# Kernel optimization log

Measured on AMD Instinct MI355X. Metric: run time of the kernel, lower is better.

## Reference

```python
import jax, jax.numpy as jnp
import numpy as np
from functools import partial

N_NODES = 10000
E_EDGES = 160000
SEQ = 32
IN_CH = 128
HID = 64
HEADS = 8
GRU_H = 256
NEG_SLOPE = 0.2


def setup_inputs() -> dict:
    key = jax.random.key(0)
    ks = jax.random.split(key, 24)
    x = jax.random.normal(ks[0], (SEQ, N_NODES, IN_CH), dtype=jnp.float32)
    edge_attr = jax.random.normal(ks[1], (E_EDGES, 3), dtype=jnp.float32)
    edge_src = jax.random.randint(ks[2], (E_EDGES,), 0, N_NODES, dtype=jnp.int32)
    # guarantee no self loops (PyG removes then re-adds them; we add them in reference)
    off = jax.random.randint(ks[3], (E_EDGES,), 1, N_NODES, dtype=jnp.int32)
    edge_dst = (edge_src + off) % N_NODES
    s = 0.05
    p = {}
    # gat1: in -> heads*hid
    p['gat1_wl'] = jax.random.normal(ks[4], (IN_CH, HEADS * HID)) * s
    p['gat1_wr'] = jax.random.normal(ks[5], (IN_CH, HEADS * HID)) * s
    p['gat1_we'] = jax.random.normal(ks[6], (3, HEADS * HID)) * s
    p['gat1_att'] = jax.random.normal(ks[7], (HEADS, HID)) * s
    p['gat1_b'] = jnp.zeros((HEADS * HID,), jnp.float32)
    # gat2: heads*hid -> 1*hid
    p['gat2_wl'] = jax.random.normal(ks[8], (HEADS * HID, HID)) * s
    p['gat2_wr'] = jax.random.normal(ks[9], (HEADS * HID, HID)) * s
    p['gat2_we'] = jax.random.normal(ks[10], (3, HID)) * s
    p['gat2_att'] = jax.random.normal(ks[11], (1, HID)) * s
    p['gat2_b'] = jnp.zeros((HID,), jnp.float32)
    # GRU layer 0, forward and backward directions (only layer 0 affects the output)
    p['gru_wih_f'] = jax.random.normal(ks[12], (3 * GRU_H, HID)) * s
    p['gru_whh_f'] = jax.random.normal(ks[13], (3 * GRU_H, GRU_H)) * s
    p['gru_bih_f'] = jnp.zeros((3 * GRU_H,), jnp.float32)
    p['gru_bhh_f'] = jnp.zeros((3 * GRU_H,), jnp.float32)
    p['gru_wih_b'] = jax.random.normal(ks[14], (3 * GRU_H, HID)) * s
    p['gru_whh_b'] = jax.random.normal(ks[15], (3 * GRU_H, GRU_H)) * s
    p['gru_bih_b'] = jnp.zeros((3 * GRU_H,), jnp.float32)
    p['gru_bhh_b'] = jnp.zeros((3 * GRU_H,), jnp.float32)
    p['fc_w'] = jax.random.normal(ks[16], (33, 2 * GRU_H)) * s
    p['fc_b'] = jnp.zeros((33,), jnp.float32)
    return dict(x=x, edge_attr=edge_attr, edge_src=edge_src, edge_dst=edge_dst, **p)


def _gatv2(x, src, dst, e_emb, wl, wr, att, b, n_nodes):
    # x: [N, F_in]; e_emb: [E_full, H, C]; att: [H, C]
    H, C = att.shape
    xl = (x @ wl).reshape(n_nodes, H, C)
    xr = (x @ wr).reshape(n_nodes, H, C)
    m = jax.nn.leaky_relu(xl[src] + xr[dst] + e_emb, NEG_SLOPE)  # [E, H, C]
    logits = jnp.einsum('ehc,hc->eh', m, att)                    # [E, H]
    mx = jax.ops.segment_max(logits, dst, num_segments=n_nodes)
    ex = jnp.exp(logits - mx[dst])
    den = jax.ops.segment_sum(ex, dst, num_segments=n_nodes)
    alpha = ex / den[dst]
    out = jax.ops.segment_sum(alpha[:, :, None] * xl[src], dst, num_segments=n_nodes)
    return out.reshape(n_nodes, H * C) + b


def _gru_scan(seq, wih, whh, bih, bhh):
    # seq: [T, N, F]; returns final hidden [N, GRU_H]
    Hh = whh.shape[1]
    def cell(h, x_t):
        gi = x_t @ wih.T + bih
        gh = h @ whh.T + bhh
        ir, iz, inn = jnp.split(gi, 3, axis=-1)
        hr, hz, hn = jnp.split(gh, 3, axis=-1)
        r = jax.nn.sigmoid(ir + hr)
        z = jax.nn.sigmoid(iz + hz)
        n = jnp.tanh(inn + r * hn)
        h = (1.0 - z) * n + z * h
        return h, None
    h0 = jnp.zeros((seq.shape[1], Hh), seq.dtype)
    hT, _ = jax.lax.scan(cell, h0, seq)
    return hT


def reference(x, edge_attr, edge_src, edge_dst,
              gat1_wl, gat1_wr, gat1_we, gat1_att, gat1_b,
              gat2_wl, gat2_wr, gat2_we, gat2_att, gat2_b,
              gru_wih_f, gru_whh_f, gru_bih_f, gru_bhh_f,
              gru_wih_b, gru_whh_b, gru_bih_b, gru_bhh_b,
              fc_w, fc_b):
    T, N, _ = x.shape
    E = edge_src.shape[0]
    loop = jnp.arange(N, dtype=edge_src.dtype)
    src = jnp.concatenate([edge_src, loop])
    dst = jnp.concatenate([edge_dst, loop])
    # self-loop edge attr = mean of incoming edge attrs (PyG fill_value='mean')
    deg = jax.ops.segment_sum(jnp.ones((E,), x.dtype), edge_dst, num_segments=N)
    loop_attr = jax.ops.segment_sum(edge_attr, edge_dst, num_segments=N) / jnp.maximum(deg, 1.0)[:, None]
    ea = jnp.concatenate([edge_attr, loop_attr], axis=0)  # [E+N, 3]
    e1 = (ea @ gat1_we).reshape(-1, HEADS, HID)
    e2 = (ea @ gat2_we).reshape(-1, 1, HID)

    @jax.checkpoint
    def step(carry, x_t):
        h1 = jax.nn.elu(_gatv2(x_t, src, dst, e1, gat1_wl, gat1_wr, gat1_att, gat1_b, N))
        h2 = jax.nn.elu(_gatv2(h1, src, dst, e2, gat2_wl, gat2_wr, gat2_att, gat2_b, N))
        return carry, h2

    _, emb = jax.lax.scan(step, 0, x)  # [T, N, HID]

    # torch code uses h_n[0] (layer-0 fwd final) and h_n[1] (layer-0 bwd final);
    # deeper GRU layers do not influence the output.
    hf = _gru_scan(emb, gru_wih_f, gru_whh_f, gru_bih_f, gru_bhh_f)
    hb = _gru_scan(emb[::-1], gru_wih_b, gru_whh_b, gru_bih_b, gru_bhh_b)
    comb = jnp.concatenate([hf, hb], axis=1)           # [N, 512]
    g = jnp.mean(comb, axis=0, keepdims=True)          # [1, 512]
    return g @ fc_w.T + fc_b                           # [1, 33]
```

## Files before the change

kernel.cpp:

```cpp
#include <hip/hip_runtime.h>

#define T_SEQ   32
#define N_NODES 10000
#define E_EDGES 160000
#define EF      (E_EDGES + N_NODES)
#define IN_CH   128
#define HID     64
#define HEADS   8
#define HC      512
#define GRU_H   256
#define G3      768

typedef __attribute__((ext_vector_type(8))) short short8;
typedef __attribute__((ext_vector_type(4))) float f32x4;
typedef unsigned short ushort_t;

__device__ __forceinline__ float wave_reduce_sum(float v){
#pragma unroll
  for (int off = 32; off; off >>= 1) v += __shfl_xor(v, off, 64);
  return v;
}

__device__ __forceinline__ ushort_t f2bf(float v){
  unsigned u = __float_as_uint(v);
  unsigned r = u + 0x7FFFu + ((u >> 16) & 1u);
  return (ushort_t)(r >> 16);
}
__device__ __forceinline__ float bf2f(ushort_t b){
  return __uint_as_float(((unsigned)b) << 16);
}

__device__ __forceinline__ void async_cp16(const void* g, void* l){
  __builtin_amdgcn_global_load_lds((const __attribute__((address_space(1))) void*)g,
                                   (__attribute__((address_space(3))) void*)l, 16, 0, 0);
}


__global__ __launch_bounds__(256)
void deg_loop_kernel(const int* __restrict__ edst, const float* __restrict__ eattr,
                     int* __restrict__ deg, float* __restrict__ lsum){
  int e = blockIdx.x * 256 + threadIdx.x;
  if (e < E_EDGES){
    int d = edst[e];
    atomicAdd(&deg[d], 1);
    atomicAdd(&lsum[d*3+0], eattr[e*3+0]);
    atomicAdd(&lsum[d*3+1], eattr[e*3+1]);
    atomicAdd(&lsum[d*3+2], eattr[e*3+2]);
  }
}

__global__ __launch_bounds__(256)
void loop_div_kernel(const int* __restrict__ deg, const float* __restrict__ lsum,
                     float* __restrict__ lattr){
  int n = blockIdx.x * 256 + threadIdx.x;
  if (n < N_NODES){
    float d = fmaxf((float)deg[n], 1.0f);
    lattr[n*3+0] = lsum[n*3+0] / d;
    lattr[n*3+1] = lsum[n*3+1] / d;
    lattr[n*3+2] = lsum[n*3+2] / d;
  }
}

__global__ __launch_bounds__(256)
void scan_rowptr_kernel(const int* __restrict__ deg, int* __restrict__ row_ptr){
  __shared__ int sums[256];
  __shared__ int base[256];
  int tid = threadIdx.x;
  const int CH = 40;
  int start = tid * CH;
  int s = 0;
  for (int k = 0; k < CH; k++){
    int n = start + k;
    if (n < N_NODES) s += deg[n];
  }
  sums[tid] = s;
  __syncthreads();
  if (tid == 0){
    int acc = 0;
    for (int i = 0; i < 256; i++){ base[i] = acc; acc += sums[i]; }
  }
  __syncthreads();
  int acc = base[tid];
  for (int k = 0; k < CH; k++){
    int n = start + k;
    if (n < N_NODES){ row_ptr[n] = acc; acc += deg[n]; }
    else if (n == N_NODES){ row_ptr[n] = acc; }
  }
}

__global__ __launch_bounds__(256)
void csr_fill_kernel(const int* __restrict__ edst, const int* __restrict__ row_ptr,
                     int* __restrict__ cursor, int* __restrict__ col){
  int e = blockIdx.x * 256 + threadIdx.x;
  if (e < E_EDGES){
    int d = edst[e];
    int pos = row_ptr[d] + atomicAdd(&cursor[d], 1);
    col[pos] = e;
  }
}

__global__ __launch_bounds__(256)
void build_emeta(const float* __restrict__ eattr, const float* __restrict__ lattr,
                 const int* __restrict__ esrc, float4* __restrict__ emeta){
  int e = blockIdx.x * 256 + threadIdx.x;
  if (e < E_EDGES){
    emeta[e] = make_float4(eattr[e*3], eattr[e*3+1], eattr[e*3+2], __int_as_float(esrc[e]));
  } else if (e < EF){
    int n = e - E_EDGES;
    emeta[e] = make_float4(lattr[n*3], lattr[n*3+1], lattr[n*3+2], __int_as_float(n));
  }
}


__global__ __launch_bounds__(256)
void split_arr4(const float4* __restrict__ src, ushort4* __restrict__ hi,
                ushort4* __restrict__ lo, long n4){
  long idx = (long)blockIdx.x * 256 + threadIdx.x;
  if (idx < n4){
    float4 v = src[idx];
    float vv[4] = {v.x, v.y, v.z, v.w};
    ushort4 h, l;
    ushort_t* hp = (ushort_t*)&h; ushort_t* lp = (ushort_t*)&l;
#pragma unroll
    for (int i = 0; i < 4; i++){
      ushort_t hh = f2bf(vv[i]);
      hp[i] = hh; lp[i] = f2bf(vv[i] - bf2f(hh));
    }
    hi[idx] = h; lo[idx] = l;
  }
}

__global__ __launch_bounds__(256)
void split_w_gat1(const float* __restrict__ wl, const float* __restrict__ wr,
                  ushort_t* __restrict__ hi, ushort_t* __restrict__ lo){
  int idx = blockIdx.x * 256 + threadIdx.x;
  if (idx >= 1024 * 128) return;
  int n = idx >> 7, k = idx & 127;
  float v = (n < 512) ? wl[k * 512 + n] : wr[k * 512 + (n - 512)];
  ushort_t h = f2bf(v);
  hi[idx] = h; lo[idx] = f2bf(v - bf2f(h));
}

__global__ __launch_bounds__(256)
void split_w_gat2(const float* __restrict__ wl, const float* __restrict__ wr,
                  ushort_t* __restrict__ hi, ushort_t* __restrict__ lo){
  int idx = blockIdx.x * 256 + threadIdx.x;
  if (idx >= 128 * 512) return;
  int n = idx >> 9, k = idx & 511;
  float v = (n < 64) ? wl[k * 64 + n] : wr[k * 64 + (n - 64)];
  ushort_t h = f2bf(v);
  hi[idx] = h; lo[idx] = f2bf(v - bf2f(h));
}

__global__ __launch_bounds__(256)
void pack_w_gru(const float* __restrict__ wih, const float* __restrict__ whh,
                ushort_t* __restrict__ hi, ushort_t* __restrict__ lo){
  int idx = blockIdx.x * 256 + threadIdx.x;
  if (idx >= 4 * 10 * 192 * 32) return;
  int kk = idx & 31;
  int r  = (idx >> 5) % 192;
  int kc = (idx >> 5) / 192 % 10;
  int jt = idx / (32 * 192 * 10);
  int g = r >> 6, jj = r & 63;
  int wrow = g * 256 + jt * 64 + jj;
  int k = kc * 32 + kk;
  float v = (k < 64) ? wih[wrow * 64 + k] : whh[wrow * 256 + (k - 64)];
  ushort_t h = f2bf(v);
  hi[idx] = h; lo[idx] = f2bf(v - bf2f(h));
}


__global__ __launch_bounds__(256)
void gemm_nolds(const ushort_t* __restrict__ Ah, const ushort_t* __restrict__ Al,
                const ushort_t* __restrict__ Bh, const ushort_t* __restrict__ Bl,
                float* __restrict__ C, int M, int K, int N){
  int tid = threadIdx.x;
  int w = tid >> 6, lane = tid & 63;
  int m16 = lane & 15, quad = lane >> 4;
  int n0 = (blockIdx.y * 4 + w) * 64;
  if (n0 >= N) return;
  int m0 = blockIdx.x * 32;

  f32x4 acc[2][4];
#pragma unroll
  for (int i = 0; i < 2; i++)
#pragma unroll
    for (int j = 0; j < 4; j++) acc[i][j] = (f32x4){0,0,0,0};

  int ar0 = m0 + m16;      if (ar0 >= M) ar0 = M - 1;
  int ar1 = m0 + 16 + m16; if (ar1 >= M) ar1 = M - 1;
  const ushort_t* Ah0 = Ah + (size_t)ar0 * K + quad * 8;
  const ushort_t* Al0 = Al + (size_t)ar0 * K + quad * 8;
  const ushort_t* Ah1 = Ah + (size_t)ar1 * K + quad * 8;
  const ushort_t* Al1 = Al + (size_t)ar1 * K + quad * 8;

  for (int k0 = 0; k0 < K; k0 += 32){
    short8 a_h[2], a_l[2];
    a_h[0] = *(const short8*)(Ah0 + k0); a_l[0] = *(const short8*)(Al0 + k0);
    a_h[1] = *(const short8*)(Ah1 + k0); a_l[1] = *(const short8*)(Al1 + k0);
#pragma unroll
    for (int nt = 0; nt < 4; nt++){
      size_t boff = (size_t)(n0 + nt * 16 + m16) * K + k0 + quad * 8;
      short8 b_h = *(const short8*)(Bh + boff);
      short8 b_l = *(const short8*)(Bl + boff);
#pragma unroll
      for (int mt = 0; mt < 2; mt++){
        acc[mt][nt] = __builtin_amdgcn_mfma_f32_16x16x32_bf16(a_h[mt], b_h, acc[mt][nt],0,0,0);
        acc[mt][nt] = __builtin_amdgcn_mfma_f32_16x16x32_bf16(a_h[mt], b_l, acc[mt][nt],0,0,0);
        acc[mt][nt] = __builtin_amdgcn_mfma_f32_16x16x32_bf16(a_l[mt], b_h, acc[mt][nt],0,0,0);
      }
    }
  }
#pragma unroll
  for (int mt = 0; mt < 2; mt++){
    int row = m0 + mt * 16 + quad * 4;
#pragma unroll
    for (int nt = 0; nt < 4; nt++){
      int cc = n0 + nt * 16 + m16;
#pragma unroll
      for (int r4 = 0; r4 < 4; r4++){
        if (row + r4 < M) C[(size_t)(row + r4) * N + cc] = acc[mt][nt][r4];
      }
    }
  }
}

__global__ __launch_bounds__(256)
void gemm1_swz(const ushort_t* __restrict__ Ah, const ushort_t* __restrict__ Al,
               const ushort_t* __restrict__ Bh, const ushort_t* __restrict__ Bl,
               float* __restrict__ C){
  const int M = N_NODES, K = IN_CH, N = 1024;
  int bid = blockIdx.x;
  int xcd = bid & 7, lk = bid >> 3;
  int wsw = (xcd < 4 ? xcd * 157 : 628 + (xcd - 4) * 156) + lk;
  int mb = wsw >> 2, nbq = wsw & 3;

  int tid = threadIdx.x;
  int w = tid >> 6, lane = tid & 63;
  int m16 = lane & 15, quad = lane >> 4;
  int n0 = (nbq * 4 + w) * 64;
  int m0 = mb * 32;

  f32x4 acc[2][4];
#pragma unroll
  for (int i = 0; i < 2; i++)
#pragma unroll
    for (int j = 0; j < 4; j++) acc[i][j] = (f32x4){0,0,0,0};

  int ar0 = m0 + m16;      if (ar0 >= M) ar0 = M - 1;
  int ar1 = m0 + 16 + m16; if (ar1 >= M) ar1 = M - 1;
  const ushort_t* Ah0 = Ah + (size_t)ar0 * K + quad * 8;
  const ushort_t* Al0 = Al + (size_t)ar0 * K + quad * 8;
  const ushort_t* Ah1 = Ah + (size_t)ar1 * K + quad * 8;
  const ushort_t* Al1 = Al + (size_t)ar1 * K + quad * 8;

  for (int k0 = 0; k0 < K; k0 += 32){
    short8 a_h[2], a_l[2];
    a_h[0] = *(const short8*)(Ah0 + k0); a_l[0] = *(const short8*)(Al0 + k0);
    a_h[1] = *(const short8*)(Ah1 + k0); a_l[1] = *(const short8*)(Al1 + k0);
#pragma unroll
    for (int nt = 0; nt < 4; nt++){
      size_t boff = (size_t)(n0 + nt * 16 + m16) * K + k0 + quad * 8;
      short8 b_h = *(const short8*)(Bh + boff);
      short8 b_l = *(const short8*)(Bl + boff);
#pragma unroll
      for (int mt = 0; mt < 2; mt++){
        acc[mt][nt] = __builtin_amdgcn_mfma_f32_16x16x32_bf16(a_h[mt], b_h, acc[mt][nt],0,0,0);
        acc[mt][nt] = __builtin_amdgcn_mfma_f32_16x16x32_bf16(a_h[mt], b_l, acc[mt][nt],0,0,0);
        acc[mt][nt] = __builtin_amdgcn_mfma_f32_16x16x32_bf16(a_l[mt], b_h, acc[mt][nt],0,0,0);
      }
    }
  }
#pragma unroll
  for (int mt = 0; mt < 2; mt++){
    int row = m0 + mt * 16 + quad * 4;
#pragma unroll
    for (int nt = 0; nt < 4; nt++){
      int cc = n0 + nt * 16 + m16;
#pragma unroll
      for (int r4 = 0; r4 < 4; r4++){
        if (row + r4 < M) C[(size_t)(row + r4) * N + cc] = acc[mt][nt][r4];
      }
    }
  }
}


struct GruArgs {
  const ushort_t *EtH[2], *EtL[2];
  const ushort_t *WpH[2], *WpL[2];
  const float    *BIH[2], *BHH[2];
  const ushort_t *HinH[2],*HinL[2];
  ushort_t *HoutH[2], *HoutL[2];
  int first;
};

#define GRU_STAGE(BB, AH, AL, ASTRIDE, ACOL, KC)                               \
  {                                                                            \
    _Pragma("unroll")                                                          \
    for (int pass = 0; pass < 2; pass++){                                      \
      int ch = pass * 256 + tid;             \
      int lch = ch ^ ((ch >> 3) & 7);              \
      int row = lch >> 2, c = (lch & 3) * 8;                                   \
      int anode = m0 + row; if (anode >= N_NODES) anode = N_NODES - 1;         \
      async_cp16(AH + (size_t)anode * ASTRIDE + (ACOL) + c, &Ah_s[BB][ch * 8]);\
      async_cp16(AL + (size_t)anode * ASTRIDE + (ACOL) + c, &Al_s[BB][ch * 8]);\
    }                                                                          \
    const ushort_t* bh = WpH + ((size_t)jt * 10 + (KC)) * 6144;                \
    const ushort_t* bl = WpL + ((size_t)jt * 10 + (KC)) * 6144;                \
    _Pragma("unroll")                                                          \
    for (int pass = 0; pass < 3; pass++){                                      \
      int ch = pass * 256 + tid;             \
      int lch = ch ^ ((ch >> 3) & 7);                                          \
      async_cp16(bh + lch * 8, &Bh_s[BB][ch * 8]);                             \
      async_cp16(bl + lch * 8, &Bl_s[BB][ch * 8]);                             \
    }                                                                          \
  }

#define GRU_COMPUTE(BB, NTGT)                                                  \
  {                                                                            \
    short8 a_h[4], a_l[4];                                                     \
    _Pragma("unroll")                                                          \
    for (int mt = 0; mt < 4; mt++){                                            \
      int r = wm * 64 + mt * 16 + m16;                                         \
      int so = ((r * 4 + quad) ^ ((r >> 1) & 7)) * 8;                          \
      a_h[mt] = *(const short8*)&Ah_s[BB][so];                                 \
      a_l[mt] = *(const short8*)&Al_s[BB][so];                                 \
    }                                                                          \
    _Pragma("unroll")                                                          \
    for (int g = 0; g < 3; g++){                                               \
      int tgt = (g < 2) ? g : (NTGT);                                          \
      _Pragma("unroll")                                                        \
      for (int nt = 0; nt < 2; nt++){                                          \
        int r = g * 64 + wn * 32 + nt * 16 + m16;                              \
        int so = ((r * 4 + quad) ^ ((r >> 1) & 7)) * 8;                        \
        short8 b_h = *(const short8*)&Bh_s[BB][so];                            \
        short8 b_l = *(const short8*)&Bl_s[BB][so];                            \
        _Pragma("unroll")                                                      \
        for (int mt = 0; mt < 4; mt++){                                        \
          acc[tgt][mt][nt] = __builtin_amdgcn_mfma_f32_16x16x32_bf16(a_h[mt], b_h, acc[tgt][mt][nt],0,0,0); \
          acc[tgt][mt][nt] = __builtin_amdgcn_mfma_f32_16x16x32_bf16(a_h[mt], b_l, acc[tgt][mt][nt],0,0,0); \
          acc[tgt][mt][nt] = __builtin_amdgcn_mfma_f32_16x16x32_bf16(a_l[mt], b_h, acc[tgt][mt][nt],0,0,0); \
        }                                                                      \
      }                                                                        \
    }                                                                          \
  }

__global__ __launch_bounds__(256, 2)
void gru_step(GruArgs ga){
  int bid = blockIdx.x;
  int wsw = (bid & 7) * 79 + (bid >> 3);
  int m0 = (wsw >> 3) * 128;
  int sub = wsw & 7;
  int jt = sub >> 1;
  int dir = sub & 1;

  const ushort_t* EtH  = ga.EtH[dir];  const ushort_t* EtL  = ga.EtL[dir];
  const ushort_t* WpH  = ga.WpH[dir];  const ushort_t* WpL  = ga.WpL[dir];
  const float*    BIH  = ga.BIH[dir];  const float*    BHH  = ga.BHH[dir];
  const ushort_t* HinH = ga.HinH[dir]; const ushort_t* HinL = ga.HinL[dir];
  ushort_t* HoutH = ga.HoutH[dir];     ushort_t* HoutL = ga.HoutL[dir];

  __shared__ __align__(16) short Ah_s[2][128 * 32];
  __shared__ __align__(16) short Al_s[2][128 * 32];
  __shared__ __align__(16) short Bh_s[2][192 * 32];
  __shared__ __align__(16) short Bl_s[2][192 * 32];

  int tid = threadIdx.x;
  int w = tid >> 6, lane = tid & 63;
  int wm = w >> 1, wn = w & 1;
  int m16 = lane & 15, quad = lane >> 4;
  int j0 = jt * 64;

  f32x4 acc[4][4][2];
#pragma unroll
  for (int g = 0; g < 4; g++)
#pragma unroll
    for (int i = 0; i < 4; i++)
#pragma unroll
      for (int j = 0; j < 2; j++) acc[g][i][j] = (f32x4){0,0,0,0};

  GRU_STAGE(0, EtH, EtL, 64, 0, 0)
  __syncthreads();
  GRU_STAGE(1, EtH, EtL, 64, 32, 1)
  GRU_COMPUTE(0, 2)
  __syncthreads();
  if (!ga.first){
    GRU_STAGE(0, HinH, HinL, 256, 0, 2)
    GRU_COMPUTE(1, 2)
    __syncthreads();
    for (int kc = 2; kc < 9; kc++){
      GRU_STAGE((kc + 1) & 1, HinH, HinL, 256, (kc - 1) * 32, kc + 1)
      GRU_COMPUTE(kc & 1, 3)
      __syncthreads();
    }
    GRU_COMPUTE(1, 3)
  } else {
    GRU_COMPUTE(1, 2)
  }

#pragma unroll
  for (int mt = 0; mt < 4; mt++){
    int row = m0 + wm * 64 + mt * 16 + quad * 4;
#pragma unroll
    for (int nt = 0; nt < 2; nt++){
      int j = j0 + wn * 32 + nt * 16 + m16;
      float br  = BIH[j] + BHH[j];
      float bz  = BIH[GRU_H + j] + BHH[GRU_H + j];
      float bni = BIH[2*GRU_H + j];
      float bnh = BHH[2*GRU_H + j];
#pragma unroll
      for (int r4 = 0; r4 < 4; r4++){
        int node = row + r4;
        if (node < N_NODES){
          float rr = 1.f / (1.f + __expf(-(acc[0][mt][nt][r4] + br)));
          float zz = 1.f / (1.f + __expf(-(acc[1][mt][nt][r4] + bz)));
          float nn = tanhf(acc[2][mt][nt][r4] + bni + rr * (acc[3][mt][nt][r4] + bnh));
          size_t hidx = (size_t)node * GRU_H + j;
          float hold = ga.first ? 0.f : (bf2f(HinH[hidx]) + bf2f(HinL[hidx]));
          float hv = (1.f - zz) * nn + zz * hold;
          ushort_t hh = f2bf(hv);
          HoutH[hidx] = hh;
          HoutL[hidx] = f2bf(hv - bf2f(hh));
        }
      }
    }
  }
}


__device__ __forceinline__ void gat1_half(float4 xl, float4 xr,
                                          float a0, float a1, float a2,
                                          float4 we0, float4 we1, float4 we2,
                                          float4 at, bool valid,
                                          float& den, float4& acc){
  float vx = xl.x + xr.x + a0*we0.x + a1*we1.x + a2*we2.x;
  float vy = xl.y + xr.y + a0*we0.y + a1*we1.y + a2*we2.y;
  float vz = xl.z + xr.z + a0*we0.z + a1*we1.z + a2*we2.z;
  float vw = xl.w + xr.w + a0*we0.w + a1*we1.w + a2*we2.w;
  vx = fmaxf(vx, 0.2f*vx); vy = fmaxf(vy, 0.2f*vy);
  vz = fmaxf(vz, 0.2f*vz); vw = fmaxf(vw, 0.2f*vw);
  float pm = vx*at.x + vy*at.y + vz*at.z + vw*at.w;
  pm += __shfl_xor(pm, 1, 64); pm += __shfl_xor(pm, 2, 64);
  pm += __shfl_xor(pm, 4, 64); pm += __shfl_xor(pm, 8, 64);
  float wgt = valid ? __expf(pm) : 0.f;
  den += wgt;
  acc.x += wgt * xl.x; acc.y += wgt * xl.y;
  acc.z += wgt * xl.z; acc.w += wgt * xl.w;
}

__global__ __launch_bounds__(256)
void gat1_fused(const float* __restrict__ xlr, const float4* __restrict__ emeta,
                const int* __restrict__ row_ptr, const int* __restrict__ col,
                const float* __restrict__ we, const float* __restrict__ att,
                const float* __restrict__ bias,
                ushort_t* __restrict__ outh, ushort_t* __restrict__ outl){
  int n = (blockIdx.x * 256 + threadIdx.x) >> 6;
  int lane = threadIdx.x & 63;
  if (n >= N_NODES) return;
  int ch0 = lane * 4;
  int ch1 = 256 + lane * 4;

  float4 att0 = *(const float4*)&att[ch0];
  float4 att1 = *(const float4*)&att[ch1];
  float4 we00 = *(const float4*)&we[ch0],        we01 = *(const float4*)&we[ch1];
  float4 we10 = *(const float4*)&we[512 + ch0],  we11 = *(const float4*)&we[512 + ch1];
  float4 we20 = *(const float4*)&we[1024 + ch0], we21 = *(const float4*)&we[1024 + ch1];
  const float* xrow_n = xlr + (size_t)n * 1024;
  float4 xr0 = *(const float4*)&xrow_n[512 + ch0];
  float4 xr1 = *(const float4*)&xrow_n[512 + ch1];

  float den0 = 0.f, den1 = 0.f;
  float4 acc0 = make_float4(0,0,0,0), acc1 = make_float4(0,0,0,0);
  int beg = row_ptr[n], end = row_ptr[n + 1];

  for (int p = beg - 1; p < end; p += 2){
    int c0 = (p >= beg) ? col[p] : (E_EDGES + n);
    bool v1 = (p + 1 < end);
    int c1 = v1 ? col[p + 1] : c0;
    float4 mt0 = emeta[c0];
    float4 mt1 = emeta[c1];
    const float* xp0 = xlr + (size_t)__float_as_int(mt0.w) * 1024;
    const float* xp1 = xlr + (size_t)__float_as_int(mt1.w) * 1024;
    float4 xa0 = *(const float4*)&xp0[ch0];
    float4 xa1 = *(const float4*)&xp0[ch1];
    float4 xb0 = *(const float4*)&xp1[ch0];
    float4 xb1 = *(const float4*)&xp1[ch1];
    gat1_half(xa0, xr0, mt0.x, mt0.y, mt0.z, we00, we10, we20, att0, true, den0, acc0);
    gat1_half(xa1, xr1, mt0.x, mt0.y, mt0.z, we01, we11, we21, att1, true, den1, acc1);
    gat1_half(xb0, xr0, mt1.x, mt1.y, mt1.z, we00, we10, we20, att0, v1, den0, acc0);
    gat1_half(xb1, xr1, mt1.x, mt1.y, mt1.z, we01, we11, we21, att1, v1, den1, acc1);
  }

  float4 b0 = *(const float4*)&bias[ch0];
  float4 b1 = *(const float4*)&bias[ch1];
  float id0 = 1.f / den0, id1 = 1.f / den1;
  float o[8];
  o[0] = acc0.x*id0 + b0.x; o[1] = acc0.y*id0 + b0.y;
  o[2] = acc0.z*id0 + b0.z; o[3] = acc0.w*id0 + b0.w;
  o[4] = acc1.x*id1 + b1.x; o[5] = acc1.y*id1 + b1.y;
  o[6] = acc1.z*id1 + b1.z; o[7] = acc1.w*id1 + b1.w;
  ushort4 h0, h1v, l0, l1v;
  ushort_t* hp0 = (ushort_t*)&h0; ushort_t* hp1 = (ushort_t*)&h1v;
  ushort_t* lp0 = (ushort_t*)&l0; ushort_t* lp1 = (ushort_t*)&l1v;
#pragma unroll
  for (int i = 0; i < 8; i++){
    float v = o[i];
    v = v > 0.f ? v : (__expf(v) - 1.f);
    ushort_t hh = f2bf(v);
    ushort_t ll = f2bf(v - bf2f(hh));
    if (i < 4){ hp0[i] = hh; lp0[i] = ll; } else { hp1[i-4] = hh; lp1[i-4] = ll; }
  }
  *(ushort4*)&outh[(size_t)n * 512 + ch0] = h0;
  *(ushort4*)&outh[(size_t)n * 512 + ch1] = h1v;
  *(ushort4*)&outl[(size_t)n * 512 + ch0] = l0;
  *(ushort4*)&outl[(size_t)n * 512 + ch1] = l1v;
}


__global__ __launch_bounds__(256)
void gat2_fused(const float* __restrict__ xlr, const float4* __restrict__ emeta,
                const int* __restrict__ row_ptr, const int* __restrict__ col,
                const float* __restrict__ we, const float* __restrict__ att,
                const float* __restrict__ bias,
                ushort_t* __restrict__ outh, ushort_t* __restrict__ outl){
  int n = (blockIdx.x * 256 + threadIdx.x) >> 6;
  int lane = threadIdx.x & 63;
  if (n >= N_NODES) return;
  int g = lane >> 4;
  int c4 = (lane & 15) * 4;

  float4 attq = *(const float4*)&att[c4];
  float4 we0q = *(const float4*)&we[c4];
  float4 we1q = *(const float4*)&we[64 + c4];
  float4 we2q = *(const float4*)&we[128 + c4];
  float4 xr4  = *(const float4*)&xlr[(size_t)n * 128 + 64 + c4];

  float den = 0.f;
  float4 acc = make_float4(0,0,0,0);
  int beg = row_ptr[n], end = row_ptr[n + 1];

  for (int p0 = beg - 1; p0 < end; p0 += 4){
    int pp = p0 + g;
    bool valid = pp < end;
    int s = n; float a0 = 0.f, a1 = 0.f, a2 = 0.f;
    if (valid){
      float4 mt = (pp < beg) ? emeta[E_EDGES + n] : emeta[col[pp]];
      a0 = mt.x; a1 = mt.y; a2 = mt.z; s = __float_as_int(mt.w);
    }
    float4 xl4 = *(const float4*)&xlr[(size_t)s * 128 + c4];
    float vx = xl4.x + xr4.x + a0*we0q.x + a1*we1q.x + a2*we2q.x;
    float vy = xl4.y + xr4.y + a0*we0q.y + a1*we1q.y + a2*we2q.y;
    float vz = xl4.z + xr4.z + a0*we0q.z + a1*we1q.z + a2*we2q.z;
    float vw = xl4.w + xr4.w + a0*we0q.w + a1*we1q.w + a2*we2q.w;
    vx = fmaxf(vx, 0.2f*vx); vy = fmaxf(vy, 0.2f*vy);
    vz = fmaxf(vz, 0.2f*vz); vw = fmaxf(vw, 0.2f*vw);
    float pm = vx*attq.x + vy*attq.y + vz*attq.z + vw*attq.w;
    pm += __shfl_xor(pm, 1, 64); pm += __shfl_xor(pm, 2, 64);
    pm += __shfl_xor(pm, 4, 64); pm += __shfl_xor(pm, 8, 64);
    float wgt = valid ? __expf(pm) : 0.f;
    den += wgt;
    acc.x += wgt * xl4.x; acc.y += wgt * xl4.y;
    acc.z += wgt * xl4.z; acc.w += wgt * xl4.w;
  }
#pragma unroll
  for (int off = 16; off <= 32; off <<= 1){
    den   += __shfl_xor(den, off, 64);
    acc.x += __shfl_xor(acc.x, off, 64);
    acc.y += __shfl_xor(acc.y, off, 64);
    acc.z += __shfl_xor(acc.z, off, 64);
    acc.w += __shfl_xor(acc.w, off, 64);
  }
  if (g == 0){
    float4 bq = *(const float4*)&bias[c4];
    float id = 1.f / den;
    float o[4];
    o[0] = acc.x*id + bq.x; o[1] = acc.y*id + bq.y;
    o[2] = acc.z*id + bq.z; o[3] = acc.w*id + bq.w;
    ushort4 hv, lv;
    ushort_t* hp = (ushort_t*)&hv; ushort_t* lp = (ushort_t*)&lv;
#pragma unroll
    for (int i = 0; i < 4; i++){
      float v = o[i];
      v = v > 0.f ? v : (__expf(v) - 1.f);
      ushort_t hh = f2bf(v);
      hp[i] = hh; lp[i] = f2bf(v - bf2f(hh));
    }
    *(ushort4*)&outh[(size_t)n * 64 + c4] = hv;
    *(ushort4*)&outl[(size_t)n * 64 + c4] = lv;
  }
}


__global__ __launch_bounds__(256)
void mean_kernel(const ushort_t* __restrict__ hfh, const ushort_t* __restrict__ hfl,
                 const ushort_t* __restrict__ hbh, const ushort_t* __restrict__ hbl,
                 float* __restrict__ g){
  int k = threadIdx.x;
  int n0 = blockIdx.x * 50;
  int n1 = n0 + 50; if (n1 > N_NODES) n1 = N_NODES;
  float sf = 0.f, sb = 0.f;
  for (int n = n0; n < n1; n++){
    size_t i = (size_t)n * GRU_H + k;
    sf += bf2f(hfh[i]) + bf2f(hfl[i]);
    sb += bf2f(hbh[i]) + bf2f(hbl[i]);
  }
  atomicAdd(&g[k], sf);
  atomicAdd(&g[GRU_H + k], sb);
}

__global__ __launch_bounds__(64)
void fc_kernel(const float* __restrict__ g, const float* __restrict__ W,
               const float* __restrict__ b, float* __restrict__ out){
  int j = blockIdx.x;
  int lane = threadIdx.x;
  float s = 0.f;
  for (int k = lane; k < 2 * GRU_H; k += 64) s += g[k] * W[j * (2 * GRU_H) + k];
  s = wave_reduce_sum(s);
  if (lane == 0) out[j] = b[j] + s * (1.0f / N_NODES);
}


extern "C" void kernel_launch(void* const* d_in, const int* in_sizes, int n_in,
                              void* d_out, int out_size, void* d_ws, size_t ws_size,
                              hipStream_t stream){
  const float* x     = (const float*)d_in[0];
  const float* eattr = (const float*)d_in[1];
  const int*   esrc  = (const int*)  d_in[2];
  const int*   edst  = (const int*)  d_in[3];
  const float* g1_wl = (const float*)d_in[4];
  const float* g1_wr = (const float*)d_in[5];
  const float* g1_we = (const float*)d_in[6];
  const float* g1_att= (const float*)d_in[7];
  const float* g1_b  = (const float*)d_in[8];
  const float* g2_wl = (const float*)d_in[9];
  const float* g2_wr = (const float*)d_in[10];
  const float* g2_we = (const float*)d_in[11];
  const float* g2_att= (const float*)d_in[12];
  const float* g2_b  = (const float*)d_in[13];
  const float* wih_f = (const float*)d_in[14];
  const float* whh_f = (const float*)d_in[15];
  const float* bih_f = (const float*)d_in[16];
  const float* bhh_f = (const float*)d_in[17];
  const float* wih_b = (const float*)d_in[18];
  const float* whh_b = (const float*)d_in[19];
  const float* bih_b = (const float*)d_in[20];
  const float* bhh_b = (const float*)d_in[21];
  const float* fc_w  = (const float*)d_in[22];
  const float* fc_b  = (const float*)d_in[23];
  float* out = (float*)d_out;

  float* ws = (float*)d_ws;
  size_t o = 0;
  auto alloc = [&](size_t nfloats) -> float* {
    float* p = ws + o; o += (nfloats + 3) & ~(size_t)3; return p;
  };
  const size_t XTOT = (size_t)T_SEQ * N_NODES * IN_CH;
  ushort_t* xh   = (ushort_t*)alloc(XTOT / 2);
  ushort_t* xlo  = (ushort_t*)alloc(XTOT / 2);
  float* xlr1    = alloc((size_t)N_NODES * 1024);
  ushort_t* h1h  = (ushort_t*)alloc((size_t)N_NODES * 512 / 2 + 4);
  ushort_t* h1l  = (ushort_t*)alloc((size_t)N_NODES * 512 / 2 + 4);
  const size_t ETOT = (size_t)T_SEQ * N_NODES * HID;
  ushort_t* embh = (ushort_t*)alloc(ETOT / 2);
  ushort_t* embl = (ushort_t*)alloc(ETOT / 2);
  const size_t HTOT = (size_t)N_NODES * GRU_H;
  ushort_t* hbuf[8];
  for (int i = 0; i < 8; i++) hbuf[i] = (ushort_t*)alloc(HTOT / 2 + 4);
  float* lsum  = alloc((size_t)N_NODES * 3);
  float* lattr = alloc((size_t)N_NODES * 3);
  float* gmean = alloc(512);
  float4* emeta = (float4*)alloc((size_t)EF * 4);
  ushort_t* W1h = (ushort_t*)alloc(1024*128/2);
  ushort_t* W1l = (ushort_t*)alloc(1024*128/2);
  ushort_t* W2h = (ushort_t*)alloc(128*512/2);
  ushort_t* W2l = (ushort_t*)alloc(128*512/2);
  const size_t WPK = 4 * 10 * 192 * 32;
  ushort_t* WpFh = (ushort_t*)alloc(WPK/2);
  ushort_t* WpFl = (ushort_t*)alloc(WPK/2);
  ushort_t* WpBh = (ushort_t*)alloc(WPK/2);
  ushort_t* WpBl = (ushort_t*)alloc(WPK/2);
  int* deg     = (int*)alloc(N_NODES + 4);
  int* row_ptr = (int*)alloc(N_NODES + 4);
  int* cursor  = (int*)alloc(N_NODES + 4);
  int* col     = (int*)alloc(E_EDGES + 4);
  float* xlr2 = xlr1;

  hipMemsetAsync(deg,    0, N_NODES * sizeof(int), stream);
  hipMemsetAsync(cursor, 0, N_NODES * sizeof(int), stream);
  hipMemsetAsync(lsum,   0, (size_t)N_NODES * 3 * sizeof(float), stream);
  hipMemsetAsync(gmean,  0, 512 * sizeof(float), stream);

  deg_loop_kernel<<<(E_EDGES + 255)/256, 256, 0, stream>>>(edst, eattr, deg, lsum);
  loop_div_kernel<<<(N_NODES + 255)/256, 256, 0, stream>>>(deg, lsum, lattr);
  scan_rowptr_kernel<<<1, 256, 0, stream>>>(deg, row_ptr);
  csr_fill_kernel<<<(E_EDGES + 255)/256, 256, 0, stream>>>(edst, row_ptr, cursor, col);
  build_emeta<<<(EF + 255)/256, 256, 0, stream>>>(eattr, lattr, esrc, emeta);
  split_arr4<<<(int)(XTOT / 4 / 256), 256, 0, stream>>>(
      (const float4*)x, (ushort4*)xh, (ushort4*)xlo, (long)(XTOT / 4));
  split_w_gat1<<<(1024*128 + 255)/256, 256, 0, stream>>>(g1_wl, g1_wr, W1h, W1l);
  split_w_gat2<<<(128*512 + 255)/256, 256, 0, stream>>>(g2_wl, g2_wr, W2h, W2l);
  pack_w_gru<<<(int)((WPK + 255)/256), 256, 0, stream>>>(wih_f, whh_f, WpFh, WpFl);
  pack_w_gru<<<(int)((WPK + 255)/256), 256, 0, stream>>>(wih_b, whh_b, WpBh, WpBl);

  const int MB32  = (N_NODES + 31) / 32;
  const int NODE_BLOCKS = (N_NODES + 3) / 4;
  for (int t = 0; t < T_SEQ; t++){
    const ushort_t* xth = xh  + (size_t)t * N_NODES * IN_CH;
    const ushort_t* xtl = xlo + (size_t)t * N_NODES * IN_CH;
    gemm1_swz<<<1252, 256, 0, stream>>>(xth, xtl, W1h, W1l, xlr1);
    gat1_fused<<<NODE_BLOCKS, 256, 0, stream>>>(
        xlr1, emeta, row_ptr, col, g1_we, g1_att, g1_b, h1h, h1l);
    gemm_nolds<<<dim3(MB32, 1), 128, 0, stream>>>(h1h, h1l, W2h, W2l, xlr2,
                                                  N_NODES, HC, 128);
    gat2_fused<<<NODE_BLOCKS, 256, 0, stream>>>(
        xlr2, emeta, row_ptr, col, g2_we, g2_att, g2_b,
        embh + (size_t)t * N_NODES * HID, embl + (size_t)t * N_NODES * HID);
  }

  {
    int fin = 0, bin = 4;
    for (int s = 0; s < T_SEQ; s++){
      int fo = fin ^ 2, bo = bin ^ 2;
      GruArgs ga;
      ga.EtH[0] = embh + (size_t)s * N_NODES * HID;
      ga.EtL[0] = embl + (size_t)s * N_NODES * HID;
      ga.EtH[1] = embh + (size_t)(T_SEQ - 1 - s) * N_NODES * HID;
      ga.EtL[1] = embl + (size_t)(T_SEQ - 1 - s) * N_NODES * HID;
      ga.WpH[0] = WpFh; ga.WpL[0] = WpFl; ga.WpH[1] = WpBh; ga.WpL[1] = WpBl;
      ga.BIH[0] = bih_f; ga.BHH[0] = bhh_f; ga.BIH[1] = bih_b; ga.BHH[1] = bhh_b;
      ga.HinH[0] = hbuf[fin];   ga.HinL[0] = hbuf[fin+1];
      ga.HinH[1] = hbuf[bin];   ga.HinL[1] = hbuf[bin+1];
      ga.HoutH[0] = hbuf[fo];   ga.HoutL[0] = hbuf[fo+1];
      ga.HoutH[1] = hbuf[bo];   ga.HoutL[1] = hbuf[bo+1];
      ga.first = (s == 0) ? 1 : 0;
      gru_step<<<632, 256, 0, stream>>>(ga);
      fin = fo; bin = bo;
    }
  }

  mean_kernel<<<(N_NODES + 49)/50, 256, 0, stream>>>(hbuf[0], hbuf[1], hbuf[4], hbuf[5], gmean);
  fc_kernel<<<33, 64, 0, stream>>>(gmean, fc_w, fc_b, out);
}
```

Before: 7.431 ms.

## Batch GAT stages over multiple timesteps per kernel launch

Each GAT stage kernel (gemm1, gat1, gemm2, gat2) now processes up to 8 timesteps per launch through blockIdx.y, using per-timestep scratch buffers sized by a workspace plan. This cuts the launch count from 128 to 16 and gives the small kernels a larger grid, most notably the 313-block gemm2. The cost is a larger workspace (xlr grows to BT×N×1024 floats), and locality per step may be worse.

After: 6.295 ms. -15.3%, faster.

```diff
diff --git a/kernel.cpp b/kernel.cpp
--- a/kernel.cpp
+++ b/kernel.cpp
@@ -171,15 +171,25 @@
 
 
 __global__ __launch_bounds__(256)
-void gemm_nolds(const ushort_t* __restrict__ Ah, const ushort_t* __restrict__ Al,
-                const ushort_t* __restrict__ Bh, const ushort_t* __restrict__ Bl,
-                float* __restrict__ C, int M, int K, int N){
+void gemm1_swz(const ushort_t* __restrict__ Ah, const ushort_t* __restrict__ Al,
+               const ushort_t* __restrict__ Bh, const ushort_t* __restrict__ Bl,
+               float* __restrict__ C){
+  const int M = N_NODES, K = IN_CH, N = 1024;
+  int tl = blockIdx.y;
+  const ushort_t* AhT = Ah + (size_t)tl * N_NODES * IN_CH;
+  const ushort_t* AlT = Al + (size_t)tl * N_NODES * IN_CH;
+  float* CT = C + (size_t)tl * N_NODES * 1024;
+
+  int bid = blockIdx.x;
+  int xcd = bid & 7, lk = bid >> 3;
+  int wsw = (xcd < 4 ? xcd * 157 : 628 + (xcd - 4) * 156) + lk;
+  int mb = wsw >> 2, nbq = wsw & 3;
+
   int tid = threadIdx.x;
   int w = tid >> 6, lane = tid & 63;
   int m16 = lane & 15, quad = lane >> 4;
-  int n0 = (blockIdx.y * 4 + w) * 64;
-  if (n0 >= N) return;
-  int m0 = blockIdx.x * 32;
+  int n0 = (nbq * 4 + w) * 64;
+  int m0 = mb * 32;
 
   f32x4 acc[2][4];
 #pragma unroll
@@ -189,10 +199,10 @@
 
   int ar0 = m0 + m16;      if (ar0 >= M) ar0 = M - 1;
   int ar1 = m0 + 16 + m16; if (ar1 >= M) ar1 = M - 1;
-  const ushort_t* Ah0 = Ah + (size_t)ar0 * K + quad * 8;
-  const ushort_t* Al0 = Al + (size_t)ar0 * K + quad * 8;
-  const ushort_t* Ah1 = Ah + (size_t)ar1 * K + quad * 8;
-  const ushort_t* Al1 = Al + (size_t)ar1 * K + quad * 8;
+  const ushort_t* Ah0 = AhT + (size_t)ar0 * K + quad * 8;
+  const ushort_t* Al0 = AlT + (size_t)ar0 * K + quad * 8;
+  const ushort_t* Ah1 = AhT + (size_t)ar1 * K + quad * 8;
+  const ushort_t* Al1 = AlT + (size_t)ar1 * K + quad * 8;
 
   for (int k0 = 0; k0 < K; k0 += 32){
     short8 a_h[2], a_l[2];
@@ -219,27 +229,28 @@
       int cc = n0 + nt * 16 + m16;
 #pragma unroll
       for (int r4 = 0; r4 < 4; r4++){
-        if (row + r4 < M) C[(size_t)(row + r4) * N + cc] = acc[mt][nt][r4];
+        if (row + r4 < M) CT[(size_t)(row + r4) * N + cc] = acc[mt][nt][r4];
       }
     }
   }
 }
 
-__global__ __launch_bounds__(256)
-void gemm1_swz(const ushort_t* __restrict__ Ah, const ushort_t* __restrict__ Al,
-               const ushort_t* __restrict__ Bh, const ushort_t* __restrict__ Bl,
-               float* __restrict__ C){
-  const int M = N_NODES, K = IN_CH, N = 1024;
-  int bid = blockIdx.x;
-  int xcd = bid & 7, lk = bid >> 3;
-  int wsw = (xcd < 4 ? xcd * 157 : 628 + (xcd - 4) * 156) + lk;
-  int mb = wsw >> 2, nbq = wsw & 3;
+
+__global__ __launch_bounds__(128)
+void gemm2_b(const ushort_t* __restrict__ Ah, const ushort_t* __restrict__ Al,
+             const ushort_t* __restrict__ Bh, const ushort_t* __restrict__ Bl,
+             float* __restrict__ C){
+  const int M = N_NODES, K = HC;
+  int tl = blockIdx.y;
+  const ushort_t* AhT = Ah + (size_t)tl * N_NODES * 512;
+  const ushort_t* AlT = Al + (size_t)tl * N_NODES * 512;
+  float* CT = C + (size_t)tl * N_NODES * 1024;
 
   int tid = threadIdx.x;
   int w = tid >> 6, lane = tid & 63;
   int m16 = lane & 15, quad = lane >> 4;
-  int n0 = (nbq * 4 + w) * 64;
-  int m0 = mb * 32;
+  int n0 = w * 64;
+  int m0 = blockIdx.x * 32;
 
   f32x4 acc[2][4];
 #pragma unroll
@@ -249,10 +260,10 @@
 
   int ar0 = m0 + m16;      if (ar0 >= M) ar0 = M - 1;
   int ar1 = m0 + 16 + m16; if (ar1 >= M) ar1 = M - 1;
-  const ushort_t* Ah0 = Ah + (size_t)ar0 * K + quad * 8;
-  const ushort_t* Al0 = Al + (size_t)ar0 * K + quad * 8;
-  const ushort_t* Ah1 = Ah + (size_t)ar1 * K + quad * 8;
-  const ushort_t* Al1 = Al + (size_t)ar1 * K + quad * 8;
+  const ushort_t* Ah0 = AhT + (size_t)ar0 * K + quad * 8;
+  const ushort_t* Al0 = AlT + (size_t)ar0 * K + quad * 8;
+  const ushort_t* Ah1 = AhT + (size_t)ar1 * K + quad * 8;
+  const ushort_t* Al1 = AlT + (size_t)ar1 * K + quad * 8;
 
   for (int k0 = 0; k0 < K; k0 += 32){
     short8 a_h[2], a_l[2];
@@ -279,7 +290,7 @@
       int cc = n0 + nt * 16 + m16;
 #pragma unroll
       for (int r4 = 0; r4 < 4; r4++){
-        if (row + r4 < M) C[(size_t)(row + r4) * N + cc] = acc[mt][nt][r4];
+        if (row + r4 < M) CT[(size_t)(row + r4) * 128 + cc] = acc[mt][nt][r4];
       }
     }
   }
@@ -450,11 +461,16 @@
 }
 
 __global__ __launch_bounds__(256)
-void gat1_fused(const float* __restrict__ xlr, const float4* __restrict__ emeta,
+void gat1_fused(const float* __restrict__ xlrb, const float4* __restrict__ emeta,
                 const int* __restrict__ row_ptr, const int* __restrict__ col,
                 const float* __restrict__ we, const float* __restrict__ att,
                 const float* __restrict__ bias,
-                ushort_t* __restrict__ outh, ushort_t* __restrict__ outl){
+                ushort_t* __restrict__ outhb, ushort_t* __restrict__ outlb){
+  int tl = blockIdx.y;
+  const float* xlr = xlrb + (size_t)tl * N_NODES * 1024;
+  ushort_t* outh = outhb + (size_t)tl * N_NODES * 512;
+  ushort_t* outl = outlb + (size_t)tl * N_NODES * 512;
+
   int n = (blockIdx.x * 256 + threadIdx.x) >> 6;
   int lane = threadIdx.x & 63;
   if (n >= N_NODES) return;
@@ -519,11 +535,15 @@
 
 
 __global__ __launch_bounds__(256)
-void gat2_fused(const float* __restrict__ xlr, const float4* __restrict__ emeta,
+void gat2_fused(const float* __restrict__ xlrb, const float4* __restrict__ emeta,
                 const int* __restrict__ row_ptr, const int* __restrict__ col,
                 const float* __restrict__ we, const float* __restrict__ att,
                 const float* __restrict__ bias,
-                ushort_t* __restrict__ outh, ushort_t* __restrict__ outl){
+                ushort_t* __restrict__ embh, ushort_t* __restrict__ embl, int t0){
+  int tl = blockIdx.y;
+  const float* xlr = xlrb + (size_t)tl * N_NODES * 1024;
+  int t = t0 + tl;
+
   int n = (blockIdx.x * 256 + threadIdx.x) >> 6;
   int lane = threadIdx.x & 63;
   if (n >= N_NODES) return;
@@ -586,8 +606,10 @@
       ushort_t hh = f2bf(v);
       hp[i] = hh; lp[i] = f2bf(v - bf2f(hh));
     }
-    *(ushort4*)&outh[(size_t)n * 64 + c4] = hv;
-    *(ushort4*)&outl[(size_t)n * 64 + c4] = lv;
+    ushort_t* oh = embh + (size_t)t * N_NODES * HID;
+    ushort_t* ol = embl + (size_t)t * N_NODES * HID;
+    *(ushort4*)&oh[(size_t)n * 64 + c4] = hv;
+    *(ushort4*)&ol[(size_t)n * 64 + c4] = lv;
   }
 }
 
@@ -650,21 +672,42 @@
   const float* fc_b  = (const float*)d_in[23];
   float* out = (float*)d_out;
 
+  const size_t XTOT = (size_t)T_SEQ * N_NODES * IN_CH;
+  const size_t ETOT = (size_t)T_SEQ * N_NODES * HID;
+  const size_t HTOT = (size_t)N_NODES * GRU_H;
+  const size_t WPK  = 4 * 10 * 192 * 32;
+
+  auto plan = [&](int bt) -> size_t {
+    size_t t = 0;
+    auto add = [&](size_t nf){ t += (nf + 3) & ~(size_t)3; };
+    add(XTOT / 2); add(XTOT / 2);
+    add((size_t)bt * N_NODES * 1024);
+    add((size_t)bt * N_NODES * 512 / 2 + 4);
+    add((size_t)bt * N_NODES * 512 / 2 + 4);
+    add(ETOT / 2); add(ETOT / 2);
+    for (int i = 0; i < 8; i++) add(HTOT / 2 + 4);
+    add((size_t)N_NODES * 3); add((size_t)N_NODES * 3); add(512);
+    add((size_t)EF * 4);
+    add(1024*128/2); add(1024*128/2); add(128*512/2); add(128*512/2);
+    for (int i = 0; i < 4; i++) add(WPK / 2);
+    add(N_NODES + 4); add(N_NODES + 4); add(N_NODES + 4); add(E_EDGES + 4);
+    return t;
+  };
+  int BT = 8;
+  while (BT > 1 && plan(BT) * sizeof(float) > ws_size) BT >>= 1;
+
   float* ws = (float*)d_ws;
   size_t o = 0;
   auto alloc = [&](size_t nfloats) -> float* {
     float* p = ws + o; o += (nfloats + 3) & ~(size_t)3; return p;
   };
-  const size_t XTOT = (size_t)T_SEQ * N_NODES * IN_CH;
   ushort_t* xh   = (ushort_t*)alloc(XTOT / 2);
   ushort_t* xlo  = (ushort_t*)alloc(XTOT / 2);
-  float* xlr1    = alloc((size_t)N_NODES * 1024);
-  ushort_t* h1h  = (ushort_t*)alloc((size_t)N_NODES * 512 / 2 + 4);
-  ushort_t* h1l  = (ushort_t*)alloc((size_t)N_NODES * 512 / 2 + 4);
-  const size_t ETOT = (size_t)T_SEQ * N_NODES * HID;
+  float* xlrb    = alloc((size_t)BT * N_NODES * 1024);
+  ushort_t* h1h  = (ushort_t*)alloc((size_t)BT * N_NODES * 512 / 2 + 4);
+  ushort_t* h1l  = (ushort_t*)alloc((size_t)BT * N_NODES * 512 / 2 + 4);
   ushort_t* embh = (ushort_t*)alloc(ETOT / 2);
   ushort_t* embl = (ushort_t*)alloc(ETOT / 2);
-  const size_t HTOT = (size_t)N_NODES * GRU_H;
   ushort_t* hbuf[8];
   for (int i = 0; i < 8; i++) hbuf[i] = (ushort_t*)alloc(HTOT / 2 + 4);
   float* lsum  = alloc((size_t)N_NODES * 3);
@@ -675,7 +718,6 @@
   ushort_t* W1l = (ushort_t*)alloc(1024*128/2);
   ushort_t* W2h = (ushort_t*)alloc(128*512/2);
   ushort_t* W2l = (ushort_t*)alloc(128*512/2);
-  const size_t WPK = 4 * 10 * 192 * 32;
   ushort_t* WpFh = (ushort_t*)alloc(WPK/2);
   ushort_t* WpFl = (ushort_t*)alloc(WPK/2);
   ushort_t* WpBh = (ushort_t*)alloc(WPK/2);
@@ -684,7 +726,6 @@
   int* row_ptr = (int*)alloc(N_NODES + 4);
   int* cursor  = (int*)alloc(N_NODES + 4);
   int* col     = (int*)alloc(E_EDGES + 4);
-  float* xlr2 = xlr1;
 
   hipMemsetAsync(deg,    0, N_NODES * sizeof(int), stream);
   hipMemsetAsync(cursor, 0, N_NODES * sizeof(int), stream);
@@ -703,19 +744,17 @@
   pack_w_gru<<<(int)((WPK + 255)/256), 256, 0, stream>>>(wih_f, whh_f, WpFh, WpFl);
   pack_w_gru<<<(int)((WPK + 255)/256), 256, 0, stream>>>(wih_b, whh_b, WpBh, WpBl);
 
-  const int MB32  = (N_NODES + 31) / 32;
+  const int MB32 = (N_NODES + 31) / 32;
   const int NODE_BLOCKS = (N_NODES + 3) / 4;
-  for (int t = 0; t < T_SEQ; t++){
-    const ushort_t* xth = xh  + (size_t)t * N_NODES * IN_CH;
-    const ushort_t* xtl = xlo + (size_t)t * N_NODES * IN_CH;
-    gemm1_swz<<<1252, 256, 0, stream>>>(xth, xtl, W1h, W1l, xlr1);
-    gat1_fused<<<NODE_BLOCKS, 256, 0, stream>>>(
-        xlr1, emeta, row_ptr, col, g1_we, g1_att, g1_b, h1h, h1l);
-    gemm_nolds<<<dim3(MB32, 1), 128, 0, stream>>>(h1h, h1l, W2h, W2l, xlr2,
-                                                  N_NODES, HC, 128);
-    gat2_fused<<<NODE_BLOCKS, 256, 0, stream>>>(
-        xlr2, emeta, row_ptr, col, g2_we, g2_att, g2_b,
-        embh + (size_t)t * N_NODES * HID, embl + (size_t)t * N_NODES * HID);
+  for (int t0 = 0; t0 < T_SEQ; t0 += BT){
+    const ushort_t* xth = xh  + (size_t)t0 * N_NODES * IN_CH;
+    const ushort_t* xtl = xlo + (size_t)t0 * N_NODES * IN_CH;
+    gemm1_swz<<<dim3(1252, BT), 256, 0, stream>>>(xth, xtl, W1h, W1l, xlrb);
+    gat1_fused<<<dim3(NODE_BLOCKS, BT), 256, 0, stream>>>(
+        xlrb, emeta, row_ptr, col, g1_we, g1_att, g1_b, h1h, h1l);
+    gemm2_b<<<dim3(MB32, BT), 128, 0, stream>>>(h1h, h1l, W2h, W2l, xlrb);
+    gat2_fused<<<dim3(NODE_BLOCKS, BT), 256, 0, stream>>>(
+        xlrb, emeta, row_ptr, col, g2_we, g2_att, g2_b, embh, embl, t0);
   }
 
   {
```
